# Kernel tuning notes

Hardware: AMD Instinct MI355X
Metric: run time of the kernel (lower is better)

Reference implementation:

```python
import jax, jax.numpy as jnp
import numpy as np
import math

B, S, HID, HEADS = 4, 1024, 1024, 16
DH = HID // HEADS


def setup_inputs() -> dict:
    key = jax.random.key(0)
    ks = jax.random.split(key, 16)
    f = lambda k, shape: jax.random.normal(k, shape, dtype=jnp.float32)
    sc = 1.0 / math.sqrt(HID)
    return {
        "q_a": f(ks[0], (B, S, HID)), "k_a": f(ks[1], (B, S, HID)), "v_a": f(ks[2], (B, S, HID)),
        "q_b": f(ks[3], (B, S, HID)), "k_b": f(ks[4], (B, S, HID)), "v_b": f(ks[5], (B, S, HID)),
        "mask": jnp.ones((B, S), dtype=jnp.int32),
        "Wa": f(ks[6], (3, HID, HID)) * sc, "ba": jnp.zeros((3, HID), jnp.float32),
        "Wb": f(ks[7], (3, HID, HID)) * sc, "bb": jnp.zeros((3, HID), jnp.float32),
        "Wo_a": f(ks[8], (HID, HID)) * sc, "bo_a": jnp.zeros((HID,), jnp.float32),
        "Wo_b": f(ks[9], (HID, HID)) * sc, "bo_b": jnp.zeros((HID,), jnp.float32),
    }


def _proj(x, W, b):
    # torch Linear: x @ W.T + b, then split heads -> [B, heads, S, dh]
    y = x @ W.T + b
    return y.reshape(x.shape[0], -1, HEADS, DH).transpose(0, 2, 1, 3)


def reference(q_a, k_a, v_a, q_b, k_b, v_b, mask, Wa, ba, Wb, bb, Wo_a, bo_a, Wo_b, bo_b):
    qa, ka, va = _proj(q_a, Wa[0], ba[0]), _proj(k_a, Wa[1], ba[1]), _proj(v_a, Wa[2], ba[2])
    qb, kb, vb = _proj(q_b, Wb[0], bb[0]), _proj(k_b, Wb[1], bb[1]), _proj(v_b, Wb[2], bb[2])
    scale = 1.0 / math.sqrt(2 * DH)
    # dual-stream score fusion: self + cross terms, all scaled by 1/sqrt(2*dh)
    corr_a = (jnp.einsum('bhqd,bhkd->bhqk', qa, ka) + jnp.einsum('bhqd,bhkd->bhqk', qa, kb)) * scale
    corr_b = (jnp.einsum('bhqd,bhkd->bhqk', qb, kb) + jnp.einsum('bhqd,bhkd->bhqk', qb, ka)) * scale
    m = (mask == 0)[:, None, None, :]  # key-padding mask broadcast over heads & queries
    corr_a = jnp.where(m, -1e9, corr_a)
    corr_b = jnp.where(m, -1e9, corr_b)
    pa = jax.nn.softmax(corr_a, axis=-1)
    pb = jax.nn.softmax(corr_b, axis=-1)
    ha = jnp.einsum('bhqk,bhkd->bhqd', pa, va).transpose(0, 2, 1, 3).reshape(q_a.shape[0], -1, HID)
    hb = jnp.einsum('bhqk,bhkd->bhqd', pb, vb).transpose(0, 2, 1, 3).reshape(q_b.shape[0], -1, HID)
    return (ha @ Wo_a.T + bo_a, hb @ Wo_b.T + bo_b)
```

## Files before the change

### kernel.cpp

```cpp
#include <hip/hip_runtime.h>


typedef __bf16 bf16;
typedef __bf16 bf16x4 __attribute__((ext_vector_type(4)));
typedef __bf16 bf16x8 __attribute__((ext_vector_type(8)));
typedef float  f32x4  __attribute__((ext_vector_type(4)));

#define HID_C   1024
#define S_C     1024
#define B_C     4
#define H_C     16
#define DH_C    64
#define NTOK    4096

__device__ __forceinline__ void gl_lds16(const bf16* g, bf16* l) {
    __builtin_amdgcn_global_load_lds(
        (const __attribute__((address_space(1))) void*)g,
        (__attribute__((address_space(3))) void*)l, 16, 0, 0);
}

struct CvtArgs {
    const float* src[10];
    bf16*        dst[10];
    int          cum[11];
};

__global__ __launch_bounds__(256) void cvt_all(CvtArgs a) {
    int blk = blockIdx.x;
    int seg = 0;
    while (blk >= a.cum[seg + 1]) ++seg;
    int i = ((blk - a.cum[seg]) * 256 + threadIdx.x) * 4;
    f32x4 v = *(const f32x4*)(a.src[seg] + i);
    *(bf16x4*)(a.dst[seg] + i) = __builtin_convertvector(v, bf16x4);
}

struct GemmJob {
    const bf16* A1; const bf16* W1;
    const bf16* A2; const bf16* W2;
    const float* bias1; const float* bias2;
    void* out; int mode; float scale;
};
struct GemmBatch { GemmJob j[5]; };

__global__ __launch_bounds__(256, 3)
void gemm_bt(GemmBatch gb) {
    const GemmJob jb = gb.j[blockIdx.z];
    const int K = HID_C;
    __shared__ bf16 a_lds[128 * 64];
    __shared__ bf16 w_lds[128 * 64];

    const int tid  = threadIdx.x;
    const int wave = tid >> 6, lane = tid & 63;
    const int quad = lane >> 4, l15 = lane & 15;
    const int swz  = l15 & 7;
    const int row0 = blockIdx.y * 128;
    const int col0 = blockIdx.x * 128;
    const int wr = (wave >> 1) * 64;
    const int wc = (wave & 1) * 64;

    f32x4 acc[4][4] = {};

    const int nkb = jb.A2 ? 32 : 16;
    for (int kb = 0; kb < nkb; ++kb) {
        const bf16* A = (kb < 16) ? jb.A1 : jb.A2;
        const bf16* W = (kb < 16) ? jb.W1 : jb.W2;
        const int k0 = (kb & 15) * 64;
        __syncthreads();
        for (int i = 0; i < 4; ++i) {
            int q = tid + i * 256;
            int r = q >> 3, c = q & 7;
            int gch = c ^ (r & 7);
            gl_lds16(A + (size_t)(row0 + r) * K + k0 + gch * 8, a_lds + q * 8);
            gl_lds16(W + (size_t)(col0 + r) * K + k0 + gch * 8, w_lds + q * 8);
        }
        __syncthreads();
        for (int kk = 0; kk < 2; ++kk) {
            const int ch = ((kk * 4 + quad) ^ swz) * 8;
            bf16x8 af[4], bw[4];
            for (int mi = 0; mi < 4; ++mi)
                af[mi] = *(const bf16x8*)(a_lds + (wr + mi * 16 + l15) * 64 + ch);
            for (int ni = 0; ni < 4; ++ni)
                bw[ni] = *(const bf16x8*)(w_lds + (wc + ni * 16 + l15) * 64 + ch);
            for (int mi = 0; mi < 4; ++mi)
                for (int ni = 0; ni < 4; ++ni)
                    acc[mi][ni] = __builtin_amdgcn_mfma_f32_16x16x32_bf16(af[mi], bw[ni], acc[mi][ni], 0, 0, 0);
        }
    }

    for (int mi = 0; mi < 4; ++mi) {
        for (int ni = 0; ni < 4; ++ni) {
            int colg = col0 + wc + ni * 16 + l15;
            float bv = jb.bias1 ? jb.bias1[colg] : 0.f;
            if (jb.bias2) bv += jb.bias2[colg];
            for (int r = 0; r < 4; ++r) {
                int rowg = row0 + wr + mi * 16 + quad * 4 + r;
                float v = (acc[mi][ni][r] + bv) * jb.scale;
                if (jb.mode == 2) {
                    ((float*)jb.out)[(size_t)rowg * HID_C + colg] = v;
                } else {
                    int b = rowg >> 10, s = rowg & 1023;
                    int h = colg >> 6,  d = colg & 63;
                    size_t idx = (jb.mode == 0)
                        ? ((size_t)((b * H_C + h) * S_C + s) * DH_C + d)
                        : ((size_t)((b * H_C + h) * DH_C + d) * S_C + s);
                    ((bf16*)jb.out)[idx] = (bf16)v;
                }
            }
        }
    }
}

__global__ __launch_bounds__(256, 2)
void attn_fused(const bf16* __restrict__ qp_a, const bf16* __restrict__ qp_b,
                const bf16* __restrict__ ksp,
                const bf16* __restrict__ vT_a, const bf16* __restrict__ vT_b,
                const int* __restrict__ mask,
                bf16* __restrict__ ho_a, bf16* __restrict__ ho_b) {
    __shared__ bf16  k_lds[2][128 * 64];
    __shared__ bf16  vT_lds[2][64 * 128];
    __shared__ float madd[1024];
    __shared__ bf16  p_lds[4 * 32 * 40];

    const int tid  = threadIdx.x;
    const int wave = tid >> 6, lane = tid & 63;
    const int quad = lane >> 4, l15 = lane & 15;
    const int swz  = l15 & 7;
    const int bh = blockIdx.x;
    const int b  = bh >> 4, h = bh & 15;
    const int s0 = blockIdx.y * 128;
    const bf16* qp   = blockIdx.z ? qp_b : qp_a;
    const bf16* vTp  = blockIdx.z ? vT_b : vT_a;
    bf16*       hout = blockIdx.z ? ho_b : ho_a;

    {
        int4 mv = *(const int4*)(mask + b * S_C + tid * 4);
        f32x4 md;
        md[0] = mv.x ? 0.f : -1e9f;
        md[1] = mv.y ? 0.f : -1e9f;
        md[2] = mv.z ? 0.f : -1e9f;
        md[3] = mv.w ? 0.f : -1e9f;
        *(f32x4*)(madd + tid * 4) = md;
    }

    bf16x8 qf[2][2];
    for (int qt = 0; qt < 2; ++qt)
        for (int kk = 0; kk < 2; ++kk)
            qf[qt][kk] = *(const bf16x8*)(qp + ((size_t)bh * S_C + s0 + wave * 32 + qt * 16 + l15) * DH_C
                                          + kk * 32 + quad * 8);

    const bf16* kbase0 = ksp + (size_t)bh * S_C * DH_C;
    const bf16* vbase0 = vTp + (size_t)bh * DH_C * S_C;
    auto stage = [&](int kt, int buf) {
        const bf16* kb = kbase0 + kt * 128 * DH_C;
        const bf16* vb = vbase0 + kt * 128;
        for (int i = 0; i < 4; ++i) {
            int q = tid + i * 256;
            int r = q >> 3, c = q & 7;
            gl_lds16(kb + r * DH_C + ((c ^ (r & 7)) * 8), &k_lds[buf][q * 8]);
            int d = q >> 4, c16 = q & 15;
            gl_lds16(vb + (size_t)d * S_C + ((c16 ^ (d & 7)) * 8), &vT_lds[buf][q * 8]);
        }
    };

    float m_i[2] = {-1e30f, -1e30f}, l_i[2] = {0.f, 0.f};
    f32x4 Oacc[2][4] = {};
    bf16* pw = p_lds + wave * (32 * 40);

    stage(0, 0);
    for (int kt = 0; kt < 8; ++kt) {
        const int cur = kt & 1;
        __syncthreads();
        if (kt < 7) stage(kt + 1, 1 - cur);
        const bf16* kl = k_lds[cur];
        const bf16* vl = vT_lds[cur];

        f32x4 sacc[8][2] = {};
        for (int kk = 0; kk < 2; ++kk) {
            const int ch = ((kk * 4 + quad) ^ swz) * 8;
            for (int ct = 0; ct < 8; ++ct) {
                bf16x8 kf = *(const bf16x8*)(kl + (ct * 16 + l15) * 64 + ch);
                sacc[ct][0] = __builtin_amdgcn_mfma_f32_16x16x32_bf16(kf, qf[0][kk], sacc[ct][0], 0, 0, 0);
                sacc[ct][1] = __builtin_amdgcn_mfma_f32_16x16x32_bf16(kf, qf[1][kk], sacc[ct][1], 0, 0, 0);
            }
        }
        for (int ct = 0; ct < 8; ++ct) {
            f32x4 md = *(const f32x4*)(madd + kt * 128 + ct * 16 + quad * 4);
            for (int qt = 0; qt < 2; ++qt)
                for (int r = 0; r < 4; ++r)
                    sacc[ct][qt][r] += md[r];
        }
        float fac[2];
        for (int qt = 0; qt < 2; ++qt) {
            float tm = sacc[0][qt][0];
            for (int ct = 0; ct < 8; ++ct)
                for (int r = 0; r < 4; ++r) tm = fmaxf(tm, sacc[ct][qt][r]);
            tm = fmaxf(tm, __shfl_xor(tm, 16, 64));
            tm = fmaxf(tm, __shfl_xor(tm, 32, 64));
            float mn = fmaxf(m_i[qt], tm);
            fac[qt] = __builtin_amdgcn_exp2f(m_i[qt] - mn);
            m_i[qt] = mn;
            float ts = 0.f;
            for (int ct = 0; ct < 8; ++ct)
                for (int r = 0; r < 4; ++r) {
                    float p = __builtin_amdgcn_exp2f(sacc[ct][qt][r] - mn);
                    sacc[ct][qt][r] = p;
                    ts += p;
                }
            ts += __shfl_xor(ts, 16, 64);
            ts += __shfl_xor(ts, 32, 64);
            l_i[qt] = l_i[qt] * fac[qt] + ts;
            for (int dt = 0; dt < 4; ++dt)
                for (int r = 0; r < 4; ++r) Oacc[qt][dt][r] *= fac[qt];
        }
        for (int c = 0; c < 4; ++c) {
            for (int qt = 0; qt < 2; ++qt)
                for (int half = 0; half < 2; ++half) {
                    bf16x4 pv = __builtin_convertvector(sacc[2 * c + half][qt], bf16x4);
                    *(bf16x4*)(pw + (qt * 16 + l15) * 40 + half * 16 + quad * 4) = pv;
                }
            bf16x8 pf0 = *(const bf16x8*)(pw + l15 * 40 + quad * 8);
            bf16x8 pf1 = *(const bf16x8*)(pw + (16 + l15) * 40 + quad * 8);
            for (int dt = 0; dt < 4; ++dt) {
                bf16x8 vf = *(const bf16x8*)(vl + (dt * 16 + l15) * 128 + ((c * 4 + quad) ^ swz) * 8);
                Oacc[0][dt] = __builtin_amdgcn_mfma_f32_16x16x32_bf16(vf, pf0, Oacc[0][dt], 0, 0, 0);
                Oacc[1][dt] = __builtin_amdgcn_mfma_f32_16x16x32_bf16(vf, pf1, Oacc[1][dt], 0, 0, 0);
            }
        }
    }

    for (int qt = 0; qt < 2; ++qt) {
        float inv = 1.f / l_i[qt];
        int token = s0 + wave * 32 + qt * 16 + l15;
        for (int dt = 0; dt < 4; ++dt) {
            f32x4 o;
            for (int r = 0; r < 4; ++r) o[r] = Oacc[qt][dt][r] * inv;
            bf16x4 ob = __builtin_convertvector(o, bf16x4);
            *(bf16x4*)(hout + (size_t)(b * S_C + token) * HID_C + h * DH_C + dt * 16 + quad * 4) = ob;
        }
    }
}

extern "C" void kernel_launch(void* const* d_in, const int* in_sizes, int n_in,
                              void* d_out, int out_size, void* d_ws, size_t ws_size,
                              hipStream_t stream) {
    const float* q_a  = (const float*)d_in[0];
    const float* k_a  = (const float*)d_in[1];
    const float* v_a  = (const float*)d_in[2];
    const float* q_b  = (const float*)d_in[3];
    const float* k_b  = (const float*)d_in[4];
    const float* v_b  = (const float*)d_in[5];
    const int*   mask = (const int*)  d_in[6];
    const float* Wa   = (const float*)d_in[7];
    const float* ba   = (const float*)d_in[8];
    const float* Wb   = (const float*)d_in[9];
    const float* bb   = (const float*)d_in[10];
    const float* Wo_a = (const float*)d_in[11];
    const float* bo_a = (const float*)d_in[12];
    const float* Wo_b = (const float*)d_in[13];
    const float* bo_b = (const float*)d_in[14];
    float* out = (float*)d_out;

    constexpr size_t ACT = (size_t)NTOK * HID_C;
    constexpr size_t W3  = 3 * (size_t)HID_C * HID_C;
    constexpr size_t W1  = (size_t)HID_C * HID_C;
    const float SC2 = 0.08838834764831845f * 1.4426950408889634f;

    bf16* w = (bf16*)d_ws;
    bf16* bfa[6];
    for (int i = 0; i < 6; ++i) bfa[i] = w + (size_t)i * ACT;
    bf16* bfWa  = w + 6 * ACT;
    bf16* bfWb  = bfWa + W3;
    bf16* bfWoA = bfWb + W3;
    bf16* bfWoB = bfWoA + W1;
    bf16* qa_p  = bfWoB + W1;
    bf16* qb_p  = qa_p + ACT;
    bf16* ks_p  = qb_p + ACT;
    bf16* vTa   = ks_p + ACT;
    bf16* vTb   = vTa + ACT;
    bf16* ha    = vTb + ACT;
    bf16* hb    = ha + ACT;

    CvtArgs ca;
    const float* srcs[10] = {q_a, k_a, v_a, q_b, k_b, v_b, Wa, Wb, Wo_a, Wo_b};
    bf16* dsts[10] = {bfa[0], bfa[1], bfa[2], bfa[3], bfa[4], bfa[5], bfWa, bfWb, bfWoA, bfWoB};
    int nblk[10] = {4096, 4096, 4096, 4096, 4096, 4096, 3072, 3072, 1024, 1024};
    int cum = 0;
    for (int i = 0; i < 10; ++i) { ca.src[i] = srcs[i]; ca.dst[i] = dsts[i]; ca.cum[i] = cum; cum += nblk[i]; }
    ca.cum[10] = cum;
    cvt_all<<<cum, 256, 0, stream>>>(ca);

    GemmBatch g1;
    g1.j[0] = { bfa[1], bfWa + W1,     bfa[4], bfWb + W1, ba + 1024, bb + 1024, ks_p, 0, 1.f  };
    g1.j[1] = { bfa[0], bfWa,          nullptr, nullptr,  ba,        nullptr,   qa_p, 0, SC2 };
    g1.j[2] = { bfa[3], bfWb,          nullptr, nullptr,  bb,        nullptr,   qb_p, 0, SC2 };
    g1.j[3] = { bfa[2], bfWa + 2 * W1, nullptr, nullptr,  ba + 2048, nullptr,   vTa,  1, 1.f  };
    g1.j[4] = { bfa[5], bfWb + 2 * W1, nullptr, nullptr,  bb + 2048, nullptr,   vTb,  1, 1.f  };
    gemm_bt<<<dim3(HID_C / 128, NTOK / 128, 5), 256, 0, stream>>>(g1);

    dim3 ga(B_C * H_C, S_C / 128, 2);
    attn_fused<<<ga, 256, 0, stream>>>(qa_p, qb_p, ks_p, vTa, vTb, mask, ha, hb);

    GemmBatch g2;
    g2.j[0] = { ha, bfWoA, nullptr, nullptr, bo_a, nullptr, (void*)out, 2, 1.f };
    g2.j[1] = { hb, bfWoB, nullptr, nullptr, bo_b, nullptr,
                (void*)(out + (size_t)NTOK * HID_C), 2, 1.f };
    g2.j[2] = g2.j[0]; g2.j[3] = g2.j[0]; g2.j[4] = g2.j[0];
    gemm_bt<<<dim3(HID_C / 128, NTOK / 128, 2), 256, 0, stream>>>(g2);
}
```

Measured before the change: 348.7 us.

## Fuse fp32-to-bf16 activation conversion into QKV projection GEMM loads

Drops the separate conversion of the six fp32 activation tensors to bf16. The projection GEMM now reads fp32 activations directly, converts them in registers and writes them to LDS, saving a full write and re-read of the bf16 activation copies. The grid is also reordered so blockIdx.x walks row tiles, which changes how blocks share weight tiles in L2. In exchange, the A-tile loads become synchronous register loads instead of async global-to-LDS copies, and A is re-read as fp32 by every column block, doubling those bytes.

```diff
diff --git a/kernel.cpp b/kernel.cpp
--- a/kernel.cpp
+++ b/kernel.cpp
@@ -20,9 +20,9 @@
 }
 
 struct CvtArgs {
-    const float* src[10];
-    bf16*        dst[10];
-    int          cum[11];
+    const float* src[4];
+    bf16*        dst[4];
+    int          cum[5];
 };
 
 __global__ __launch_bounds__(256) void cvt_all(CvtArgs a) {
@@ -35,10 +35,10 @@
 }
 
 struct GemmJob {
-    const bf16* A1; const bf16* W1;
-    const bf16* A2; const bf16* W2;
+    const void* A1; const bf16* W1;
+    const void* A2; const bf16* W2;
     const float* bias1; const float* bias2;
-    void* out; int mode; float scale;
+    void* out; int mode; int a_f32; float scale;
 };
 struct GemmBatch { GemmJob j[5]; };
 
@@ -53,8 +53,8 @@
     const int wave = tid >> 6, lane = tid & 63;
     const int quad = lane >> 4, l15 = lane & 15;
     const int swz  = l15 & 7;
-    const int row0 = blockIdx.y * 128;
-    const int col0 = blockIdx.x * 128;
+    const int row0 = blockIdx.x * 128;
+    const int col0 = blockIdx.y * 128;
     const int wr = (wave >> 1) * 64;
     const int wc = (wave & 1) * 64;
 
@@ -62,16 +62,35 @@
 
     const int nkb = jb.A2 ? 32 : 16;
     for (int kb = 0; kb < nkb; ++kb) {
-        const bf16* A = (kb < 16) ? jb.A1 : jb.A2;
+        const void* A = (kb < 16) ? jb.A1 : jb.A2;
         const bf16* W = (kb < 16) ? jb.W1 : jb.W2;
         const int k0 = (kb & 15) * 64;
         __syncthreads();
         for (int i = 0; i < 4; ++i) {
             int q = tid + i * 256;
             int r = q >> 3, c = q & 7;
-            int gch = c ^ (r & 7);
-            gl_lds16(A + (size_t)(row0 + r) * K + k0 + gch * 8, a_lds + q * 8);
-            gl_lds16(W + (size_t)(col0 + r) * K + k0 + gch * 8, w_lds + q * 8);
+            gl_lds16(W + (size_t)(col0 + r) * K + k0 + ((c ^ (r & 7)) * 8), w_lds + q * 8);
+        }
+        if (jb.a_f32) {
+            const float* Af = (const float*)A;
+            for (int i = 0; i < 4; ++i) {
+                int q = tid + i * 256;
+                int r = q >> 3, c = q & 7;
+                const float* src = Af + (size_t)(row0 + r) * K + k0 + ((c ^ (r & 7)) * 8);
+                f32x4 lo = *(const f32x4*)src;
+                f32x4 hi = *(const f32x4*)(src + 4);
+                bf16x4 l4 = __builtin_convertvector(lo, bf16x4);
+                bf16x4 h4 = __builtin_convertvector(hi, bf16x4);
+                bf16x8 v8 = __builtin_shufflevector(l4, h4, 0, 1, 2, 3, 4, 5, 6, 7);
+                *(bf16x8*)(a_lds + q * 8) = v8;
+            }
+        } else {
+            const bf16* Ab = (const bf16*)A;
+            for (int i = 0; i < 4; ++i) {
+                int q = tid + i * 256;
+                int r = q >> 3, c = q & 7;
+                gl_lds16(Ab + (size_t)(row0 + r) * K + k0 + ((c ^ (r & 7)) * 8), a_lds + q * 8);
+            }
         }
         __syncthreads();
         for (int kk = 0; kk < 2; ++kk) {
@@ -266,9 +285,7 @@
     const float SC2 = 0.08838834764831845f * 1.4426950408889634f;
 
     bf16* w = (bf16*)d_ws;
-    bf16* bfa[6];
-    for (int i = 0; i < 6; ++i) bfa[i] = w + (size_t)i * ACT;
-    bf16* bfWa  = w + 6 * ACT;
+    bf16* bfWa  = w;
     bf16* bfWb  = bfWa + W3;
     bf16* bfWoA = bfWb + W3;
     bf16* bfWoB = bfWoA + W1;
@@ -281,29 +298,29 @@
     bf16* hb    = ha + ACT;
 
     CvtArgs ca;
-    const float* srcs[10] = {q_a, k_a, v_a, q_b, k_b, v_b, Wa, Wb, Wo_a, Wo_b};
-    bf16* dsts[10] = {bfa[0], bfa[1], bfa[2], bfa[3], bfa[4], bfa[5], bfWa, bfWb, bfWoA, bfWoB};
-    int nblk[10] = {4096, 4096, 4096, 4096, 4096, 4096, 3072, 3072, 1024, 1024};
+    const float* srcs[4] = {Wa, Wb, Wo_a, Wo_b};
+    bf16* dsts[4] = {bfWa, bfWb, bfWoA, bfWoB};
+    int nblk[4] = {3072, 3072, 1024, 1024};
     int cum = 0;
-    for (int i = 0; i < 10; ++i) { ca.src[i] = srcs[i]; ca.dst[i] = dsts[i]; ca.cum[i] = cum; cum += nblk[i]; }
-    ca.cum[10] = cum;
+    for (int i = 0; i < 4; ++i) { ca.src[i] = srcs[i]; ca.dst[i] = dsts[i]; ca.cum[i] = cum; cum += nblk[i]; }
+    ca.cum[4] = cum;
     cvt_all<<<cum, 256, 0, stream>>>(ca);
 
     GemmBatch g1;
-    g1.j[0] = { bfa[1], bfWa + W1,     bfa[4], bfWb + W1, ba + 1024, bb + 1024, ks_p, 0, 1.f  };
-    g1.j[1] = { bfa[0], bfWa,          nullptr, nullptr,  ba,        nullptr,   qa_p, 0, SC2 };
-    g1.j[2] = { bfa[3], bfWb,          nullptr, nullptr,  bb,        nullptr,   qb_p, 0, SC2 };
-    g1.j[3] = { bfa[2], bfWa + 2 * W1, nullptr, nullptr,  ba + 2048, nullptr,   vTa,  1, 1.f  };
-    g1.j[4] = { bfa[5], bfWb + 2 * W1, nullptr, nullptr,  bb + 2048, nullptr,   vTb,  1, 1.f  };
-    gemm_bt<<<dim3(HID_C / 128, NTOK / 128, 5), 256, 0, stream>>>(g1);
+    g1.j[0] = { k_a, bfWa + W1,     k_b,     bfWb + W1, ba + 1024, bb + 1024, ks_p, 0, 1, 1.f  };
+    g1.j[1] = { q_a, bfWa,          nullptr, nullptr,   ba,        nullptr,   qa_p, 0, 1, SC2 };
+    g1.j[2] = { q_b, bfWb,          nullptr, nullptr,   bb,        nullptr,   qb_p, 0, 1, SC2 };
+    g1.j[3] = { v_a, bfWa + 2 * W1, nullptr, nullptr,   ba + 2048, nullptr,   vTa,  1, 1, 1.f  };
+    g1.j[4] = { v_b, bfWb + 2 * W1, nullptr, nullptr,   bb + 2048, nullptr,   vTb,  1, 1, 1.f  };
+    gemm_bt<<<dim3(NTOK / 128, HID_C / 128, 5), 256, 0, stream>>>(g1);
 
     dim3 ga(B_C * H_C, S_C / 128, 2);
     attn_fused<<<ga, 256, 0, stream>>>(qa_p, qb_p, ks_p, vTa, vTb, mask, ha, hb);
 
     GemmBatch g2;
-    g2.j[0] = { ha, bfWoA, nullptr, nullptr, bo_a, nullptr, (void*)out, 2, 1.f };
+    g2.j[0] = { ha, bfWoA, nullptr, nullptr, bo_a, nullptr, (void*)out, 2, 0, 1.f };
     g2.j[1] = { hb, bfWoB, nullptr, nullptr, bo_b, nullptr,
-                (void*)(out + (size_t)NTOK * HID_C), 2, 1.f };
+                (void*)(out + (size_t)NTOK * HID_C), 2, 0, 1.f };
     g2.j[2] = g2.j[0]; g2.j[3] = g2.j[0]; g2.j[4] = g2.j[0];
-    gemm_bt<<<dim3(HID_C / 128, NTOK / 128, 2), 256, 0, stream>>>(g2);
-}
+    gemm_bt<<<dim3(NTOK / 128, HID_C / 128, 2), 256, 0, stream>>>(g2);
+}
```

Result: no change. 352.4 us (+1.1%).
